# Kernel optimization log

Measured on AMD Instinct MI355X. Metric: run time of the kernel, lower is better.

Reference implementation:

```python
import jax, jax.numpy as jnp
import numpy as np

VOCAB = 32000
WORDVEC = 256
HIDDEN = 512
NULL_TOKEN = 0


def setup_inputs() -> dict:
    key = jax.random.key(0)
    ks = jax.random.split(key, 8)
    N, Tp1 = 16, 257
    captions = jax.random.randint(ks[0], (N, Tp1), 0, VOCAB, dtype=jnp.int64 if jax.config.jax_enable_x64 else jnp.int32)
    W_embed = jax.random.normal(ks[1], (VOCAB, WORDVEC), jnp.float32) / 100.0
    Wx = jax.random.normal(ks[2], (WORDVEC, 4 * HIDDEN), jnp.float32) / np.sqrt(WORDVEC).astype(np.float32)
    Wh = jax.random.normal(ks[3], (HIDDEN, 4 * HIDDEN), jnp.float32) / np.sqrt(HIDDEN).astype(np.float32)
    b = jnp.zeros((4 * HIDDEN,), jnp.float32)
    W_vocab = jax.random.normal(ks[4], (HIDDEN, VOCAB), jnp.float32) / np.sqrt(HIDDEN).astype(np.float32)
    b_vocab = jnp.zeros((VOCAB,), jnp.float32)
    h_init = jax.random.normal(ks[5], (HIDDEN,), jnp.float32)
    return {"captions": captions, "W_embed": W_embed, "Wx": Wx, "Wh": Wh,
            "b": b, "W_vocab": W_vocab, "b_vocab": b_vocab, "h_init": h_init}


def reference(captions, W_embed, Wx, Wh, b, W_vocab, b_vocab, h_init):
    cap_in = captions[:, :-1]   # [N, T]
    cap_out = captions[:, 1:]   # [N, T]
    mask = (cap_out != NULL_TOKEN).astype(jnp.float32)
    N = cap_in.shape[0]
    H = h_init.shape[0]

    # Embedding lookup: [N, T, D]
    x = W_embed[cap_in]
    # Precompute input projections as one big GEMM: [T, N, 4H]
    xw = jnp.einsum('ntd,dk->tnk', x, Wx) + b

    h0 = jnp.tile(h_init, (N, 1))          # [N, H]
    c0 = jnp.zeros_like(h0)                 # lstm_forward starts c at zeros

    def step(carry, a_x):
        h, c = carry
        a = a_x + h @ Wh                    # [N, 4H]
        i, f, o, g = jnp.split(a, 4, axis=-1)
        i = jax.nn.sigmoid(i)
        f = jax.nn.sigmoid(f)
        o = jax.nn.sigmoid(o)
        g = jnp.tanh(g)
        c = f * c + i * g
        h = o * jnp.tanh(c)
        return (h, c), h

    _, hs = jax.lax.scan(step, (h0, c0), xw)  # hs: [T, N, H]

    # Temporal affine: [N, T, V]
    logits = jnp.einsum('tnh,hv->ntv', hs, W_vocab) + b_vocab
    logp = jax.nn.log_softmax(logits, axis=-1)
    nll = -jnp.take_along_axis(logp, cap_out[..., None], axis=-1)[..., 0]
    loss = jnp.sum(nll * mask) / N
    return loss
```

## Files before the change

### kernel.cpp

```cpp
#include <hip/hip_runtime.h>

#define VOCAB   32000
#define WORDVEC 256
#define HIDDEN  512
#define TSTEPS  256
#define NBATCH  16
#define NROWS   (TSTEPS*NBATCH)
#define GATES   (4*HIDDEN)
#define NVB     125
#define NWG     32

typedef __attribute__((ext_vector_type(8))) short short8;
typedef __attribute__((ext_vector_type(4))) float f32x4;
typedef unsigned long long u64;

__device__ __forceinline__ unsigned short f2bf(float x){
    union { float f; unsigned int u; } v; v.f = x;
    unsigned int r = v.u + 0x7fffu + ((v.u >> 16) & 1u);
    return (unsigned short)(r >> 16);
}

__global__ __launch_bounds__(256) void wv_pack(const float* __restrict__ Wv, unsigned short* __restrict__ WvP){
    __shared__ float s[64][65];
    int v0 = blockIdx.x * 64;
    int k0 = blockIdx.y * 64;
    int tid = threadIdx.x;
    for (int i = 0; i < 16; ++i){
        int lin = tid + i*256;
        int kk = lin >> 6, vv = lin & 63;
        s[kk][vv] = Wv[(long)(k0+kk)*VOCAB + v0 + vv];
    }
    __syncthreads();
    for (int i = 0; i < 2; ++i){
        int lr = tid + i*256;
        int f  = lr >> 6;
        int vbl = f >> 1, ktl = f & 1;
        int L = lr & 63, q = L >> 4, ln = L & 15;
        short8 o;
        #pragma unroll
        for (int j = 0; j < 8; ++j)
            o[j] = (short)f2bf(s[ktl*32 + q*8 + j][vbl*16 + ln]);
        long vb = blockIdx.x*4 + vbl;
        long kt = blockIdx.y*2 + ktl;
        *(short8*)(WvP + ((vb*16 + kt)*64 + L)*8) = o;
    }
}

__global__ void whp_prep(const float* __restrict__ Wh, unsigned short* __restrict__ Whp){
    int w = blockIdx.x; int tid = threadIdx.x;
    for (int item = tid; item < 4096; item += 256){
        int f = item >> 6;
        int L = item & 63;
        int kt = f >> 2, nt = f & 3;
        int q = L >> 4, ln = L & 15;
        int col = nt*HIDDEN + w*16 + ln;
        short8 vvec;
        for (int jj = 0; jj < 8; ++jj){
            int k = kt*32 + q*8 + jj;
            vvec[jj] = (short)f2bf(Wh[(long)k*GATES + col]);
        }
        *(short8*)(Whp + ((long)w*4096 + item)*8) = vvec;
    }
}

__global__ void hg_init(const float* __restrict__ h_init, u64* __restrict__ hx){
    int p = blockIdx.x*256 + threadIdx.x;
    int fq = p >> 6;
    int j  = (p & 3) * 2;
    int u0 = (fq>>2)*32 + (fq&3)*8 + j;
    u64 pk = (u64)f2bf(h_init[u0]) | ((u64)f2bf(h_init[u0+1]) << 16);
    hx[p] = pk;
}

__global__ __launch_bounds__(256) void embed_xw(const int* __restrict__ captions,
        const float* __restrict__ Wemb, const float* __restrict__ Wx,
        const float* __restrict__ b, float* __restrict__ xw){
    __shared__ float xs[8][WORDVEC];
    __shared__ int toks[8];
    int tid = threadIdx.x;
    int r0 = blockIdx.x * 8;
    if (tid < 8){
        int r = r0 + tid; int t = r >> 4, n = r & 15;
        toks[tid] = captions[n*257 + t];
    }
    __syncthreads();
    for (int i = 0; i < 8; ++i){
        int lin = tid + i*256;
        int ri = lin >> 8, d = lin & 255;
        xs[ri][d] = Wemb[(long)toks[ri]*WORDVEC + d];
    }
    __syncthreads();
    float4 b0 = *(const float4*)(b + tid*4);
    float4 b1 = *(const float4*)(b + 1024 + tid*4);
    float acc[8][8];
    for (int ri = 0; ri < 8; ++ri){
        acc[ri][0]=b0.x; acc[ri][1]=b0.y; acc[ri][2]=b0.z; acc[ri][3]=b0.w;
        acc[ri][4]=b1.x; acc[ri][5]=b1.y; acc[ri][6]=b1.z; acc[ri][7]=b1.w;
    }
    for (int d = 0; d < WORDVEC; ++d){
        float4 w0 = *(const float4*)(Wx + (long)d*GATES + tid*4);
        float4 w1 = *(const float4*)(Wx + (long)d*GATES + 1024 + tid*4);
        #pragma unroll
        for (int ri = 0; ri < 8; ++ri){
            float xv = xs[ri][d];
            acc[ri][0] += xv*w0.x; acc[ri][1] += xv*w0.y;
            acc[ri][2] += xv*w0.z; acc[ri][3] += xv*w0.w;
            acc[ri][4] += xv*w1.x; acc[ri][5] += xv*w1.y;
            acc[ri][6] += xv*w1.z; acc[ri][7] += xv*w1.w;
        }
    }
    for (int ri = 0; ri < 8; ++ri){
        float4 o0 = {acc[ri][0],acc[ri][1],acc[ri][2],acc[ri][3]};
        float4 o1 = {acc[ri][4],acc[ri][5],acc[ri][6],acc[ri][7]};
        *(float4*)(xw + (long)(r0+ri)*GATES + tid*4) = o0;
        *(float4*)(xw + (long)(r0+ri)*GATES + 1024 + tid*4) = o1;
    }
}

__global__ __launch_bounds__(256) void lstm_mfma(const float* __restrict__ xw,
        const unsigned short* __restrict__ Whp, u64* __restrict__ hx,
        unsigned short* __restrict__ hsP){
    __shared__ unsigned int hstage[4096];
    __shared__ float a_s[4][16][16];
    int w = blockIdx.x;
    int tid = threadIdx.x;
    int wv = tid >> 6;
    int L = tid & 63;
    int q = L >> 4, ln = L & 15;
    int s_idx = tid >> 4, jl = tid & 15;

    short8 bw[16];
    #pragma unroll
    for (int kt = 0; kt < 16; ++kt)
        bw[kt] = *(const short8*)(Whp + ((long)w*4096 + (kt*4+wv)*64 + L)*8);

    float c_r = 0.f;
    int fq_pub = (w>>1)*4 + (w&1)*2 + (jl>>3);
    int pubIdx = fq_pub*64 + s_idx*4 + ((jl>>1)&3);
    int kt_h = w >> 1;
    int q_h  = ((w & 1) << 1) | (jl >> 3);
    int j_h  = jl & 7;

    for (int t = 0; t < TSTEPS; ++t){
        long xb = (long)(t*16 + s_idx)*GATES + w*16 + jl;
        float xg0 = xw[xb], xg1 = xw[xb+512], xg2 = xw[xb+1024], xg3 = xw[xb+1536];

        const u64* hr = hx + (t & 1)*4096;
        u64*       hw = hx + ((t+1) & 1)*4096;

        u64 v[16];
        #pragma unroll
        for (int i = 0; i < 16; ++i)
            v[i] = __hip_atomic_load(hr + tid + i*256, __ATOMIC_RELAXED, __HIP_MEMORY_SCOPE_AGENT);
        for (;;){
            u64 bad = 0;
            #pragma unroll
            for (int i = 0; i < 16; ++i) bad |= (v[i] >> 32) ^ (u64)(unsigned)t;
            if (!bad) break;
            #pragma unroll
            for (int i = 0; i < 16; ++i)
                v[i] = __hip_atomic_load(hr + tid + i*256, __ATOMIC_RELAXED, __HIP_MEMORY_SCOPE_AGENT);
        }
        #pragma unroll
        for (int i = 0; i < 16; ++i) hstage[tid + i*256] = (unsigned)v[i];
        __syncthreads();

        f32x4 acc = {0.f,0.f,0.f,0.f};
        #pragma unroll
        for (int kt = 0; kt < 16; ++kt){
            short8 a = *(const short8*)((const unsigned short*)hstage + (kt*256 + q*64 + ln*4)*2);
            acc = __builtin_amdgcn_mfma_f32_16x16x32_bf16(a, bw[kt], acc, 0, 0, 0);
        }
        #pragma unroll
        for (int r = 0; r < 4; ++r) a_s[wv][q*4 + r][ln] = acc[r];
        __syncthreads();

        float ai = a_s[0][s_idx][jl] + xg0;
        float af = a_s[1][s_idx][jl] + xg1;
        float ao = a_s[2][s_idx][jl] + xg2;
        float ag = a_s[3][s_idx][jl] + xg3;
        float ig = 1.f/(1.f + __expf(-ai));
        float fg = 1.f/(1.f + __expf(-af));
        float og = 1.f/(1.f + __expf(-ao));
        float gg = 2.f/(1.f + __expf(-2.f*ag)) - 1.f;
        c_r = fg*c_r + ig*gg;
        float hv = og * (2.f/(1.f + __expf(-2.f*c_r)) - 1.f);
        unsigned short hb = f2bf(hv);

        int hv32 = (int)hb;
        int other = __shfl(hv32, L ^ 1);
        if ((jl & 1) == 0){
            u64 pk = (u64)(unsigned short)hv32
                   | ((u64)(unsigned short)other << 16)
                   | ((u64)(unsigned)(t+1) << 32);
            __hip_atomic_store(hw + pubIdx, pk, __ATOMIC_RELAXED, __HIP_MEMORY_SCOPE_AGENT);
        }
        int rb = s_idx*16 + (t >> 4);
        hsP[(((long)(rb*16 + kt_h))*64 + q_h*16 + (t & 15))*8 + j_h] = hb;
    }
}

__global__ __launch_bounds__(256) void vocab_gemm(const unsigned short* __restrict__ hsP,
        const unsigned short* __restrict__ WvP, const float* __restrict__ bvoc,
        const int* __restrict__ captions, float* __restrict__ pmax,
        float* __restrict__ psum, float* __restrict__ tlog){
    int bm = blockIdx.x;
    int bn = blockIdx.y;
    int tid = threadIdx.x;
    int wv = tid >> 6, L = tid & 63;
    int q = L >> 4, ln = L & 15;
    __shared__ int   tgt_s[64];
    __shared__ float wmax_s[4][64], wsum_s[4][64];
    if (tid < 64){
        int rg = bm*64 + tid;
        tgt_s[tid] = captions[(rg >> 8)*257 + (rg & 255) + 1];
    }
    __syncthreads();
    f32x4 acc[4][4];
    for (int mt=0;mt<4;++mt) for (int nt=0;nt<4;++nt) acc[mt][nt] = (f32x4){0.f,0.f,0.f,0.f};
    int colb = bn*256 + wv*64;
    const unsigned short* aB = hsP + ((long)(bm*4)*16)*512;
    const unsigned short* bB = WvP + ((long)(bn*16 + wv*4)*16)*512;
    #pragma unroll 4
    for (int kt = 0; kt < 16; ++kt){
        short8 a[4], bb[4];
        #pragma unroll
        for (int mt=0;mt<4;++mt)
            a[mt] = *(const short8*)(aB + ((long)(mt*16 + kt)*64 + L)*8);
        #pragma unroll
        for (int nt=0;nt<4;++nt)
            bb[nt] = *(const short8*)(bB + ((long)(nt*16 + kt)*64 + L)*8);
        #pragma unroll
        for (int mt=0;mt<4;++mt)
            #pragma unroll
            for (int nt=0;nt<4;++nt)
                acc[mt][nt] = __builtin_amdgcn_mfma_f32_16x16x32_bf16(a[mt], bb[nt], acc[mt][nt], 0,0,0);
    }
    float bv[4];
    #pragma unroll
    for (int nt=0;nt<4;++nt) bv[nt] = bvoc[colb + nt*16 + ln];
    #pragma unroll
    for (int mt=0;mt<4;++mt) for (int nt=0;nt<4;++nt) for (int r=0;r<4;++r)
        acc[mt][nt][r] += bv[nt];
    #pragma unroll
    for (int mt=0;mt<4;++mt) for (int r=0;r<4;++r){
        int rl = mt*16 + q*4 + r;
        int tg = tgt_s[rl] - colb;
        if (tg >= 0 && tg < 64){
            int nt = tg >> 4;
            if ((tg & 15) == ln) tlog[bm*64 + rl] = acc[mt][nt][r];
        }
    }
    #pragma unroll
    for (int mt=0;mt<4;++mt){
        #pragma unroll
        for (int r=0;r<4;++r){
            float m = fmaxf(fmaxf(acc[mt][0][r],acc[mt][1][r]), fmaxf(acc[mt][2][r],acc[mt][3][r]));
            for (int d=1; d<16; d<<=1) m = fmaxf(m, __shfl_xor(m, d, 16));
            float s = __expf(acc[mt][0][r]-m) + __expf(acc[mt][1][r]-m)
                    + __expf(acc[mt][2][r]-m) + __expf(acc[mt][3][r]-m);
            for (int d=1; d<16; d<<=1) s += __shfl_xor(s, d, 16);
            if (ln == 0){ int rl = mt*16 + q*4 + r; wmax_s[wv][rl] = m; wsum_s[wv][rl] = s; }
        }
    }
    __syncthreads();
    if (tid < 64){
        float M = fmaxf(fmaxf(wmax_s[0][tid],wmax_s[1][tid]), fmaxf(wmax_s[2][tid],wmax_s[3][tid]));
        float S = 0.f;
        for (int ww=0; ww<4; ++ww) S += wsum_s[ww][tid]*__expf(wmax_s[ww][tid]-M);
        pmax[(long)bn*NROWS + bm*64 + tid] = M;
        psum[(long)bn*NROWS + bm*64 + tid] = S;
    }
}

__global__ __launch_bounds__(256) void reduce_loss(const float* __restrict__ pmax,
        const float* __restrict__ psum, const float* __restrict__ tlog,
        const int* __restrict__ captions, float* __restrict__ out){
    int r = blockIdx.x*256 + threadIdx.x;
    float M = -1e30f;
    for (int p=0;p<NVB;++p) M = fmaxf(M, pmax[(long)p*NROWS + r]);
    float S = 0.f;
    for (int p=0;p<NVB;++p) S += psum[(long)p*NROWS + r]*__expf(pmax[(long)p*NROWS + r]-M);
    float lse = M + logf(S);
    float nll = lse - tlog[r];
    int tok = captions[(r >> 8)*257 + (r & 255) + 1];
    float val = (tok != 0) ? nll : 0.f;
    __shared__ float red[256];
    red[threadIdx.x] = val; __syncthreads();
    for (int s=128; s>0; s>>=1){
        if (threadIdx.x < s) red[threadIdx.x] += red[threadIdx.x+s];
        __syncthreads();
    }
    if (threadIdx.x == 0) atomicAdd(out, red[0] * (1.0f/16.0f));
}

extern "C" void kernel_launch(void* const* d_in, const int* in_sizes, int n_in,
                              void* d_out, int out_size, void* d_ws, size_t ws_size,
                              hipStream_t stream){
    const int*   captions = (const int*)  d_in[0];
    const float* Wemb     = (const float*)d_in[1];
    const float* Wx       = (const float*)d_in[2];
    const float* Wh       = (const float*)d_in[3];
    const float* b        = (const float*)d_in[4];
    const float* Wv       = (const float*)d_in[5];
    const float* bvoc     = (const float*)d_in[6];
    const float* h_init   = (const float*)d_in[7];

    char* ws = (char*)d_ws;
    float*          xw   = (float*)         (ws + 0);
    unsigned short* WvP  = (unsigned short*)(ws + 33554432);
    unsigned short* hsP  = (unsigned short*)(ws + 66322432);
    float*          pmax = (float*)         (ws + 70516736);
    float*          psum = (float*)         (ws + 72564736);
    float*          tlog = (float*)         (ws + 74612736);
    unsigned short* Whp  = (unsigned short*)(ws + 74629120);
    u64*            hx   = (u64*)           (ws + 76726272);

    float* out_f = (float*)d_out;

    (void)hipMemsetAsync(d_out, 0, sizeof(float), stream);

    hipLaunchKernelGGL(wv_pack,      dim3(500, 8), dim3(256), 0, stream, Wv, WvP);
    hipLaunchKernelGGL(whp_prep,     dim3(NWG),    dim3(256), 0, stream, Wh, Whp);
    hipLaunchKernelGGL(hg_init,      dim3(16),     dim3(256), 0, stream, h_init, hx);
    hipLaunchKernelGGL(embed_xw,     dim3(512),    dim3(256), 0, stream, captions, Wemb, Wx, b, xw);
    hipLaunchKernelGGL(lstm_mfma,    dim3(NWG),    dim3(256), 0, stream, xw, Whp, hx, hsP);
    hipLaunchKernelGGL(vocab_gemm,   dim3(64,NVB), dim3(256), 0, stream, hsP, WvP, bvoc, captions, pmax, psum, tlog);
    hipLaunchKernelGGL(reduce_loss,  dim3(16),     dim3(256), 0, stream, pmax, psum, tlog, captions, out_f);
}
```

Before: 1.147 ms.

## Overlap vocab GEMM with LSTM recurrence via progress flags and merge prep kernels

Merges the four setup kernels into one prep_all launch. Folds the vocab GEMM into the LSTM kernel as extra blocks that spin on per-workgroup progress counters, so logits for finished timestep chunks are computed while the recurrence is still running. The LSTM blocks now write hidden states with atomic stores and publish a counter every 16 steps. The intent is to hide the serial recurrence latency behind GEMM work and to cut launch overhead. The risks are that the 32 LSTM blocks may not get scheduled ahead of the spinning vocab blocks (guarded only by a spin cap), and that vocab blocks sharing CUs can slow the latency-critical recurrence.

New measurement: 1.169 ms. About the same (+1.9%).

```diff
diff --git a/kernel.cpp b/kernel.cpp
--- a/kernel.cpp
+++ b/kernel.cpp
@@ -9,10 +9,14 @@
 #define GATES   (4*HIDDEN)
 #define NVB     125
 #define NWG     32
+#define NVBLK   8000
+#define SPINCAP (1<<16)
 
 typedef __attribute__((ext_vector_type(8))) short short8;
 typedef __attribute__((ext_vector_type(4))) float f32x4;
 typedef unsigned long long u64;
+
+#define AGLOAD(p) __hip_atomic_load((p), __ATOMIC_RELAXED, __HIP_MEMORY_SCOPE_AGENT)
 
 __device__ __forceinline__ unsigned short f2bf(float x){
     union { float f; unsigned int u; } v; v.f = x;
@@ -20,110 +24,206 @@
     return (unsigned short)(r >> 16);
 }
 
-__global__ __launch_bounds__(256) void wv_pack(const float* __restrict__ Wv, unsigned short* __restrict__ WvP){
+__global__ __launch_bounds__(256) void prep_all(const int* __restrict__ captions,
+        const float* __restrict__ Wemb, const float* __restrict__ Wx,
+        const float* __restrict__ b, float* __restrict__ xw,
+        const float* __restrict__ Wh, unsigned short* __restrict__ Whp,
+        const float* __restrict__ h_init, u64* __restrict__ hx,
+        const float* __restrict__ Wv, unsigned short* __restrict__ WvP,
+        int* __restrict__ prog){
     __shared__ float s[64][65];
-    int v0 = blockIdx.x * 64;
-    int k0 = blockIdx.y * 64;
+    float (*xs)[WORDVEC] = (float(*)[WORDVEC])s;
+    __shared__ int toks[8];
+    int bid = blockIdx.x;
     int tid = threadIdx.x;
-    for (int i = 0; i < 16; ++i){
-        int lin = tid + i*256;
-        int kk = lin >> 6, vv = lin & 63;
-        s[kk][vv] = Wv[(long)(k0+kk)*VOCAB + v0 + vv];
+    if (bid < 512){
+        int r0 = bid * 8;
+        if (tid < 8){
+            int r = r0 + tid; int t = r >> 4, n = r & 15;
+            toks[tid] = captions[n*257 + t];
+        }
+        __syncthreads();
+        for (int i = 0; i < 8; ++i){
+            int lin = tid + i*256;
+            int ri = lin >> 8, d = lin & 255;
+            xs[ri][d] = Wemb[(long)toks[ri]*WORDVEC + d];
+        }
+        __syncthreads();
+        float4 b0 = *(const float4*)(b + tid*4);
+        float4 b1 = *(const float4*)(b + 1024 + tid*4);
+        float acc[8][8];
+        for (int ri = 0; ri < 8; ++ri){
+            acc[ri][0]=b0.x; acc[ri][1]=b0.y; acc[ri][2]=b0.z; acc[ri][3]=b0.w;
+            acc[ri][4]=b1.x; acc[ri][5]=b1.y; acc[ri][6]=b1.z; acc[ri][7]=b1.w;
+        }
+        for (int d = 0; d < WORDVEC; ++d){
+            float4 w0 = *(const float4*)(Wx + (long)d*GATES + tid*4);
+            float4 w1 = *(const float4*)(Wx + (long)d*GATES + 1024 + tid*4);
+            #pragma unroll
+            for (int ri = 0; ri < 8; ++ri){
+                float xv = xs[ri][d];
+                acc[ri][0] += xv*w0.x; acc[ri][1] += xv*w0.y;
+                acc[ri][2] += xv*w0.z; acc[ri][3] += xv*w0.w;
+                acc[ri][4] += xv*w1.x; acc[ri][5] += xv*w1.y;
+                acc[ri][6] += xv*w1.z; acc[ri][7] += xv*w1.w;
+            }
+        }
+        for (int ri = 0; ri < 8; ++ri){
+            float4 o0 = {acc[ri][0],acc[ri][1],acc[ri][2],acc[ri][3]};
+            float4 o1 = {acc[ri][4],acc[ri][5],acc[ri][6],acc[ri][7]};
+            *(float4*)(xw + (long)(r0+ri)*GATES + tid*4) = o0;
+            *(float4*)(xw + (long)(r0+ri)*GATES + 1024 + tid*4) = o1;
+        }
+    } else if (bid < 544){
+        int w = bid - 512;
+        for (int item = tid; item < 4096; item += 256){
+            int f = item >> 6;
+            int L = item & 63;
+            int kt = f >> 2, nt = f & 3;
+            int q = L >> 4, ln = L & 15;
+            int col = nt*HIDDEN + w*16 + ln;
+            short8 vvec;
+            for (int jj = 0; jj < 8; ++jj){
+                int k = kt*32 + q*8 + jj;
+                vvec[jj] = (short)f2bf(Wh[(long)k*GATES + col]);
+            }
+            *(short8*)(Whp + ((long)w*4096 + item)*8) = vvec;
+        }
+    } else if (bid < 560){
+        if (bid == 544 && tid < 32) prog[tid] = 0;
+        int p = (bid - 544)*256 + tid;
+        int fq = p >> 6;
+        int j  = (p & 3) * 2;
+        int u0 = (fq>>2)*32 + (fq&3)*8 + j;
+        u64 pk = (u64)f2bf(h_init[u0]) | ((u64)f2bf(h_init[u0+1]) << 16);
+        hx[p] = pk;
+    } else {
+        int tile = bid - 560;
+        int v0 = (tile >> 3) * 64;
+        int k0 = (tile & 7) * 64;
+        for (int i = 0; i < 16; ++i){
+            int lin = tid + i*256;
+            int kk = lin >> 6, vv = lin & 63;
+            s[kk][vv] = Wv[(long)(k0+kk)*VOCAB + v0 + vv];
+        }
+        __syncthreads();
+        for (int i = 0; i < 2; ++i){
+            int lr = tid + i*256;
+            int f  = lr >> 6;
+            int vbl = f >> 1, ktl = f & 1;
+            int L = lr & 63, q = L >> 4, ln = L & 15;
+            short8 o;
+            #pragma unroll
+            for (int j = 0; j < 8; ++j)
+                o[j] = (short)f2bf(s[ktl*32 + q*8 + j][vbl*16 + ln]);
+            long vb = (long)(tile >> 3)*4 + vbl;
+            long kt = (long)(tile & 7)*2 + ktl;
+            *(short8*)(WvP + ((vb*16 + kt)*64 + L)*8) = o;
+        }
     }
-    __syncthreads();
-    for (int i = 0; i < 2; ++i){
-        int lr = tid + i*256;
-        int f  = lr >> 6;
-        int vbl = f >> 1, ktl = f & 1;
-        int L = lr & 63, q = L >> 4, ln = L & 15;
-        short8 o;
-        #pragma unroll
-        for (int j = 0; j < 8; ++j)
-            o[j] = (short)f2bf(s[ktl*32 + q*8 + j][vbl*16 + ln]);
-        long vb = blockIdx.x*4 + vbl;
-        long kt = blockIdx.y*2 + ktl;
-        *(short8*)(WvP + ((vb*16 + kt)*64 + L)*8) = o;
-    }
-}
-
-__global__ void whp_prep(const float* __restrict__ Wh, unsigned short* __restrict__ Whp){
-    int w = blockIdx.x; int tid = threadIdx.x;
-    for (int item = tid; item < 4096; item += 256){
-        int f = item >> 6;
-        int L = item & 63;
-        int kt = f >> 2, nt = f & 3;
-        int q = L >> 4, ln = L & 15;
-        int col = nt*HIDDEN + w*16 + ln;
-        short8 vvec;
-        for (int jj = 0; jj < 8; ++jj){
-            int k = kt*32 + q*8 + jj;
-            vvec[jj] = (short)f2bf(Wh[(long)k*GATES + col]);
-        }
-        *(short8*)(Whp + ((long)w*4096 + item)*8) = vvec;
-    }
-}
-
-__global__ void hg_init(const float* __restrict__ h_init, u64* __restrict__ hx){
-    int p = blockIdx.x*256 + threadIdx.x;
-    int fq = p >> 6;
-    int j  = (p & 3) * 2;
-    int u0 = (fq>>2)*32 + (fq&3)*8 + j;
-    u64 pk = (u64)f2bf(h_init[u0]) | ((u64)f2bf(h_init[u0+1]) << 16);
-    hx[p] = pk;
-}
-
-__global__ __launch_bounds__(256) void embed_xw(const int* __restrict__ captions,
-        const float* __restrict__ Wemb, const float* __restrict__ Wx,
-        const float* __restrict__ b, float* __restrict__ xw){
-    __shared__ float xs[8][WORDVEC];
-    __shared__ int toks[8];
-    int tid = threadIdx.x;
-    int r0 = blockIdx.x * 8;
-    if (tid < 8){
-        int r = r0 + tid; int t = r >> 4, n = r & 15;
-        toks[tid] = captions[n*257 + t];
-    }
-    __syncthreads();
-    for (int i = 0; i < 8; ++i){
-        int lin = tid + i*256;
-        int ri = lin >> 8, d = lin & 255;
-        xs[ri][d] = Wemb[(long)toks[ri]*WORDVEC + d];
-    }
-    __syncthreads();
-    float4 b0 = *(const float4*)(b + tid*4);
-    float4 b1 = *(const float4*)(b + 1024 + tid*4);
-    float acc[8][8];
-    for (int ri = 0; ri < 8; ++ri){
-        acc[ri][0]=b0.x; acc[ri][1]=b0.y; acc[ri][2]=b0.z; acc[ri][3]=b0.w;
-        acc[ri][4]=b1.x; acc[ri][5]=b1.y; acc[ri][6]=b1.z; acc[ri][7]=b1.w;
-    }
-    for (int d = 0; d < WORDVEC; ++d){
-        float4 w0 = *(const float4*)(Wx + (long)d*GATES + tid*4);
-        float4 w1 = *(const float4*)(Wx + (long)d*GATES + 1024 + tid*4);
-        #pragma unroll
-        for (int ri = 0; ri < 8; ++ri){
-            float xv = xs[ri][d];
-            acc[ri][0] += xv*w0.x; acc[ri][1] += xv*w0.y;
-            acc[ri][2] += xv*w0.z; acc[ri][3] += xv*w0.w;
-            acc[ri][4] += xv*w1.x; acc[ri][5] += xv*w1.y;
-            acc[ri][6] += xv*w1.z; acc[ri][7] += xv*w1.w;
-        }
-    }
-    for (int ri = 0; ri < 8; ++ri){
-        float4 o0 = {acc[ri][0],acc[ri][1],acc[ri][2],acc[ri][3]};
-        float4 o1 = {acc[ri][4],acc[ri][5],acc[ri][6],acc[ri][7]};
-        *(float4*)(xw + (long)(r0+ri)*GATES + tid*4) = o0;
-        *(float4*)(xw + (long)(r0+ri)*GATES + 1024 + tid*4) = o1;
-    }
-}
-
-__global__ __launch_bounds__(256) void lstm_mfma(const float* __restrict__ xw,
+}
+
+__global__ __launch_bounds__(256, 2) void lstm_vocab(const float* __restrict__ xw,
         const unsigned short* __restrict__ Whp, u64* __restrict__ hx,
-        unsigned short* __restrict__ hsP){
+        unsigned short* __restrict__ hsP, int* __restrict__ prog,
+        const unsigned short* __restrict__ WvP, const float* __restrict__ bvoc,
+        const int* __restrict__ captions, float* __restrict__ pmax,
+        float* __restrict__ psum, float* __restrict__ tlog){
     __shared__ unsigned int hstage[4096];
     __shared__ float a_s[4][16][16];
+    __shared__ int   tgt_s[64];
+    __shared__ float wmax_s[4][64], wsum_s[4][64];
+    int tid = threadIdx.x;
+
+    if (blockIdx.x >= NWG){
+        int vid = blockIdx.x - NWG;
+        int pri = vid / 2000;
+        int idx = vid % 2000;
+        int bn  = idx % 125;
+        int bm  = (idx / 125) * 4 + pri;
+        int need = (pri + 1) * 4;
+
+        if (tid == 0){
+            int cnt = 0;
+            for (;;){
+                int mn = 1 << 30;
+                for (int i = 0; i < 32; ++i){
+                    int p = AGLOAD(&prog[i]);
+                    mn = p < mn ? p : mn;
+                }
+                if (mn >= need) break;
+                __builtin_amdgcn_s_sleep(32);
+                if (++cnt > SPINCAP) break;
+            }
+        }
+        __syncthreads();
+
+        int wv = tid >> 6, L = tid & 63;
+        int q = L >> 4, ln = L & 15;
+        if (tid < 64){
+            int rg = bm*64 + tid;
+            tgt_s[tid] = captions[(rg >> 8)*257 + (rg & 255) + 1];
+        }
+        __syncthreads();
+        f32x4 acc[4][4];
+        for (int mt=0;mt<4;++mt) for (int nt=0;nt<4;++nt) acc[mt][nt] = (f32x4){0.f,0.f,0.f,0.f};
+        int colb = bn*256 + wv*64;
+        const unsigned short* aB = hsP + ((long)(bm*4)*16)*512;
+        const unsigned short* bB = WvP + ((long)(bn*16 + wv*4)*16)*512;
+        #pragma unroll 4
+        for (int kt = 0; kt < 16; ++kt){
+            short8 a[4], bb[4];
+            #pragma unroll
+            for (int mt=0;mt<4;++mt)
+                a[mt] = *(const short8*)(aB + ((long)(mt*16 + kt)*64 + L)*8);
+            #pragma unroll
+            for (int nt=0;nt<4;++nt)
+                bb[nt] = *(const short8*)(bB + ((long)(nt*16 + kt)*64 + L)*8);
+            #pragma unroll
+            for (int mt=0;mt<4;++mt)
+                #pragma unroll
+                for (int nt=0;nt<4;++nt)
+                    acc[mt][nt] = __builtin_amdgcn_mfma_f32_16x16x32_bf16(a[mt], bb[nt], acc[mt][nt], 0,0,0);
+        }
+        float bv[4];
+        #pragma unroll
+        for (int nt=0;nt<4;++nt) bv[nt] = bvoc[colb + nt*16 + ln];
+        #pragma unroll
+        for (int mt=0;mt<4;++mt) for (int nt=0;nt<4;++nt) for (int r=0;r<4;++r)
+            acc[mt][nt][r] += bv[nt];
+        #pragma unroll
+        for (int mt=0;mt<4;++mt) for (int r=0;r<4;++r){
+            int rl = mt*16 + q*4 + r;
+            int tg = tgt_s[rl] - colb;
+            if (tg >= 0 && tg < 64){
+                int nt = tg >> 4;
+                if ((tg & 15) == ln) tlog[bm*64 + rl] = acc[mt][nt][r];
+            }
+        }
+        #pragma unroll
+        for (int mt=0;mt<4;++mt){
+            #pragma unroll
+            for (int r=0;r<4;++r){
+                float m = fmaxf(fmaxf(acc[mt][0][r],acc[mt][1][r]), fmaxf(acc[mt][2][r],acc[mt][3][r]));
+                for (int d=1; d<16; d<<=1) m = fmaxf(m, __shfl_xor(m, d, 16));
+                float s = __expf(acc[mt][0][r]-m) + __expf(acc[mt][1][r]-m)
+                        + __expf(acc[mt][2][r]-m) + __expf(acc[mt][3][r]-m);
+                for (int d=1; d<16; d<<=1) s += __shfl_xor(s, d, 16);
+                if (ln == 0){ int rl = mt*16 + q*4 + r; wmax_s[wv][rl] = m; wsum_s[wv][rl] = s; }
+            }
+        }
+        __syncthreads();
+        if (tid < 64){
+            float M = fmaxf(fmaxf(wmax_s[0][tid],wmax_s[1][tid]), fmaxf(wmax_s[2][tid],wmax_s[3][tid]));
+            float S = 0.f;
+            for (int ww=0; ww<4; ++ww) S += wsum_s[ww][tid]*__expf(wmax_s[ww][tid]-M);
+            pmax[(long)bn*NROWS + bm*64 + tid] = M;
+            psum[(long)bn*NROWS + bm*64 + tid] = S;
+        }
+        return;
+    }
+
     int w = blockIdx.x;
-    int tid = threadIdx.x;
     int wv = tid >> 6;
     int L = tid & 63;
     int q = L >> 4, ln = L & 15;
@@ -140,6 +240,7 @@
     int kt_h = w >> 1;
     int q_h  = ((w & 1) << 1) | (jl >> 3);
     int j_h  = jl & 7;
+    unsigned int* hsP32 = (unsigned int*)hsP;
 
     for (int t = 0; t < TSTEPS; ++t){
         long xb = (long)(t*16 + s_idx)*GATES + w*16 + jl;
@@ -151,7 +252,7 @@
         u64 v[16];
         #pragma unroll
         for (int i = 0; i < 16; ++i)
-            v[i] = __hip_atomic_load(hr + tid + i*256, __ATOMIC_RELAXED, __HIP_MEMORY_SCOPE_AGENT);
+            v[i] = AGLOAD(hr + tid + i*256);
         for (;;){
             u64 bad = 0;
             #pragma unroll
@@ -159,7 +260,7 @@
             if (!bad) break;
             #pragma unroll
             for (int i = 0; i < 16; ++i)
-                v[i] = __hip_atomic_load(hr + tid + i*256, __ATOMIC_RELAXED, __HIP_MEMORY_SCOPE_AGENT);
+                v[i] = AGLOAD(hr + tid + i*256);
         }
         #pragma unroll
         for (int i = 0; i < 16; ++i) hstage[tid + i*256] = (unsigned)v[i];
@@ -189,87 +290,23 @@
 
         int hv32 = (int)hb;
         int other = __shfl(hv32, L ^ 1);
+        int rb = s_idx*16 + (t >> 4);
         if ((jl & 1) == 0){
             u64 pk = (u64)(unsigned short)hv32
                    | ((u64)(unsigned short)other << 16)
                    | ((u64)(unsigned)(t+1) << 32);
             __hip_atomic_store(hw + pubIdx, pk, __ATOMIC_RELAXED, __HIP_MEMORY_SCOPE_AGENT);
-        }
-        int rb = s_idx*16 + (t >> 4);
-        hsP[(((long)(rb*16 + kt_h))*64 + q_h*16 + (t & 15))*8 + j_h] = hb;
-    }
-}
-
-__global__ __launch_bounds__(256) void vocab_gemm(const unsigned short* __restrict__ hsP,
-        const unsigned short* __restrict__ WvP, const float* __restrict__ bvoc,
-        const int* __restrict__ captions, float* __restrict__ pmax,
-        float* __restrict__ psum, float* __restrict__ tlog){
-    int bm = blockIdx.x;
-    int bn = blockIdx.y;
-    int tid = threadIdx.x;
-    int wv = tid >> 6, L = tid & 63;
-    int q = L >> 4, ln = L & 15;
-    __shared__ int   tgt_s[64];
-    __shared__ float wmax_s[4][64], wsum_s[4][64];
-    if (tid < 64){
-        int rg = bm*64 + tid;
-        tgt_s[tid] = captions[(rg >> 8)*257 + (rg & 255) + 1];
-    }
-    __syncthreads();
-    f32x4 acc[4][4];
-    for (int mt=0;mt<4;++mt) for (int nt=0;nt<4;++nt) acc[mt][nt] = (f32x4){0.f,0.f,0.f,0.f};
-    int colb = bn*256 + wv*64;
-    const unsigned short* aB = hsP + ((long)(bm*4)*16)*512;
-    const unsigned short* bB = WvP + ((long)(bn*16 + wv*4)*16)*512;
-    #pragma unroll 4
-    for (int kt = 0; kt < 16; ++kt){
-        short8 a[4], bb[4];
-        #pragma unroll
-        for (int mt=0;mt<4;++mt)
-            a[mt] = *(const short8*)(aB + ((long)(mt*16 + kt)*64 + L)*8);
-        #pragma unroll
-        for (int nt=0;nt<4;++nt)
-            bb[nt] = *(const short8*)(bB + ((long)(nt*16 + kt)*64 + L)*8);
-        #pragma unroll
-        for (int mt=0;mt<4;++mt)
-            #pragma unroll
-            for (int nt=0;nt<4;++nt)
-                acc[mt][nt] = __builtin_amdgcn_mfma_f32_16x16x32_bf16(a[mt], bb[nt], acc[mt][nt], 0,0,0);
-    }
-    float bv[4];
-    #pragma unroll
-    for (int nt=0;nt<4;++nt) bv[nt] = bvoc[colb + nt*16 + ln];
-    #pragma unroll
-    for (int mt=0;mt<4;++mt) for (int nt=0;nt<4;++nt) for (int r=0;r<4;++r)
-        acc[mt][nt][r] += bv[nt];
-    #pragma unroll
-    for (int mt=0;mt<4;++mt) for (int r=0;r<4;++r){
-        int rl = mt*16 + q*4 + r;
-        int tg = tgt_s[rl] - colb;
-        if (tg >= 0 && tg < 64){
-            int nt = tg >> 4;
-            if ((tg & 15) == ln) tlog[bm*64 + rl] = acc[mt][nt][r];
-        }
-    }
-    #pragma unroll
-    for (int mt=0;mt<4;++mt){
-        #pragma unroll
-        for (int r=0;r<4;++r){
-            float m = fmaxf(fmaxf(acc[mt][0][r],acc[mt][1][r]), fmaxf(acc[mt][2][r],acc[mt][3][r]));
-            for (int d=1; d<16; d<<=1) m = fmaxf(m, __shfl_xor(m, d, 16));
-            float s = __expf(acc[mt][0][r]-m) + __expf(acc[mt][1][r]-m)
-                    + __expf(acc[mt][2][r]-m) + __expf(acc[mt][3][r]-m);
-            for (int d=1; d<16; d<<=1) s += __shfl_xor(s, d, 16);
-            if (ln == 0){ int rl = mt*16 + q*4 + r; wmax_s[wv][rl] = m; wsum_s[wv][rl] = s; }
-        }
-    }
-    __syncthreads();
-    if (tid < 64){
-        float M = fmaxf(fmaxf(wmax_s[0][tid],wmax_s[1][tid]), fmaxf(wmax_s[2][tid],wmax_s[3][tid]));
-        float S = 0.f;
-        for (int ww=0; ww<4; ++ww) S += wsum_s[ww][tid]*__expf(wmax_s[ww][tid]-M);
-        pmax[(long)bn*NROWS + bm*64 + tid] = M;
-        psum[(long)bn*NROWS + bm*64 + tid] = S;
+            unsigned int hp = (unsigned int)(unsigned short)hv32
+                            | ((unsigned int)(unsigned short)other << 16);
+            __hip_atomic_store(hsP32 + (((long)(rb*16 + kt_h))*64 + q_h*16 + (t & 15))*4 + (j_h >> 1),
+                               hp, __ATOMIC_RELAXED, __HIP_MEMORY_SCOPE_AGENT);
+        }
+        if ((t & 15) == 15){
+            asm volatile("s_waitcnt vmcnt(0)" ::: "memory");
+            __syncthreads();
+            if (tid == 0)
+                __hip_atomic_store(&prog[w], (t >> 4) + 1, __ATOMIC_RELAXED, __HIP_MEMORY_SCOPE_AGENT);
+        }
     }
 }
 
@@ -315,16 +352,16 @@
     float*          tlog = (float*)         (ws + 74612736);
     unsigned short* Whp  = (unsigned short*)(ws + 74629120);
     u64*            hx   = (u64*)           (ws + 76726272);
+    int*            prog = (int*)           (ws + 76791808);
 
     float* out_f = (float*)d_out;
 
     (void)hipMemsetAsync(d_out, 0, sizeof(float), stream);
 
-    hipLaunchKernelGGL(wv_pack,      dim3(500, 8), dim3(256), 0, stream, Wv, WvP);
-    hipLaunchKernelGGL(whp_prep,     dim3(NWG),    dim3(256), 0, stream, Wh, Whp);
-    hipLaunchKernelGGL(hg_init,      dim3(16),     dim3(256), 0, stream, h_init, hx);
-    hipLaunchKernelGGL(embed_xw,     dim3(512),    dim3(256), 0, stream, captions, Wemb, Wx, b, xw);
-    hipLaunchKernelGGL(lstm_mfma,    dim3(NWG),    dim3(256), 0, stream, xw, Whp, hx, hsP);
-    hipLaunchKernelGGL(vocab_gemm,   dim3(64,NVB), dim3(256), 0, stream, hsP, WvP, bvoc, captions, pmax, psum, tlog);
-    hipLaunchKernelGGL(reduce_loss,  dim3(16),     dim3(256), 0, stream, pmax, psum, tlog, captions, out_f);
-}
+    hipLaunchKernelGGL(prep_all,    dim3(4560),       dim3(256), 0, stream,
+                       captions, Wemb, Wx, b, xw, Wh, Whp, h_init, hx, Wv, WvP, prog);
+    hipLaunchKernelGGL(lstm_vocab,  dim3(NWG+NVBLK),  dim3(256), 0, stream,
+                       xw, Whp, hx, hsP, prog, WvP, bvoc, captions, pmax, psum, tlog);
+    hipLaunchKernelGGL(reduce_loss, dim3(16),         dim3(256), 0, stream,
+                       pmax, psum, tlog, captions, out_f);
+}
```
